# Performance work log

Hardware: AMD Instinct MI355X
Metric: run time of the kernel (lower is better)

## Reference

```python
import jax, jax.numpy as jnp
import numpy as np

NUM_HEADS = 4
KEY_DIMS = 32  # c // num_heads


def rel_to_abs(x):
    # x: [B, N, W, 2W-1] relative logits -> [B, N, W, W] absolute logits
    b, n, w, _ = x.shape
    x = jnp.pad(x, ((0, 0), (0, 0), (0, 0), (0, 1)))           # [b,n,w,2w]
    x = x.reshape(b, n, w * 2 * w)
    x = jnp.pad(x, ((0, 0), (0, 0), (0, w - 1)))
    x = x.reshape(b, n, w + 1, 2 * w - 1)
    return x[:, :, :w, w - 1:]


def rel_logits_1d(q, rel_k):
    # q: [B, heads, X, Y, d], rel_k: [2Y-1, d] -> [B, heads, X, X, Y, Y]
    b, nh, xx, yy, d = q.shape
    rl = jnp.einsum('bhxyd,md->bhxym', q, rel_k)               # [b,h,x,y,2y-1]
    rl = rel_to_abs(rl.reshape(b, nh * xx, yy, 2 * yy - 1))    # [b,h*x,y,y]
    rl = rl.reshape(b, nh, xx, 1, yy, yy)
    return jnp.broadcast_to(rl, (b, nh, xx, xx, yy, yy))


def relative_position_bias(pos_q, pos_emb_h, pos_emb_w):
    # pos_q: [B, heads, H, W, d] -> bias [B, heads, H, W, H, W]
    rw = rel_logits_1d(pos_q, pos_emb_w)                        # [b,h,H,H,W,W]
    rw = rw.transpose(0, 1, 2, 4, 3, 5)                         # [b,h,H,W,H,W]
    rh = rel_logits_1d(pos_q.transpose(0, 1, 3, 2, 4), pos_emb_h)  # [b,h,W,W,H,H]
    rh = rh.transpose(0, 1, 4, 2, 5, 3)                         # [b,h,H,W,H,W]
    return rw + rh


def setup_inputs() -> dict:
    key = jax.random.key(0)
    k1, k2, k3, k4 = jax.random.split(key, 4)
    B, H, W, C = 2, 64, 64, 128
    qk_dims = NUM_HEADS * KEY_DIMS  # 128
    out_channels = C
    x = jax.random.normal(k1, (B, H, W, C), dtype=jnp.float32)
    w_qkv = jax.random.normal(k2, (C, 2 * qk_dims + out_channels), dtype=jnp.float32) * 0.05
    pos_emb_h = jax.random.normal(k3, (2 * H - 1, KEY_DIMS), dtype=jnp.float32) * 0.05
    pos_emb_w = jax.random.normal(k4, (2 * W - 1, KEY_DIMS), dtype=jnp.float32) * 0.05
    return {'x': x, 'w_qkv': w_qkv, 'pos_emb_h': pos_emb_h, 'pos_emb_w': pos_emb_w}


def reference(x, w_qkv, pos_emb_h, pos_emb_w):
    B, H, W, C = x.shape
    nh, kd = NUM_HEADS, KEY_DIMS
    qk_dims = nh * kd
    oc = C
    scale = 1.0 / float(kd) ** 0.5

    qkv = jnp.einsum('bhwc,cd->bhwd', x, w_qkv)                 # 1x1 conv, no bias
    q, k, v = jnp.split(qkv, [qk_dims, 2 * qk_dims], axis=-1)
    L = H * W
    q = q.reshape(B, L, nh, kd).transpose(0, 2, 1, 3)           # [B,nh,L,kd]
    k = k.reshape(B, L, nh, kd).transpose(0, 2, 1, 3)           # [B,nh,L,kd]
    v = v.reshape(B, L, nh, oc // nh).transpose(0, 2, 1, 3)     # [B,nh,L,dv]

    pos_q = q.reshape(B, nh, H, W, kd)
    pos = relative_position_bias(pos_q, pos_emb_h, pos_emb_w).reshape(B, nh, L, L)

    scores = jnp.einsum('bnqd,bnkd->bnqk', q, k) * scale + pos  # [B,nh,L,L]
    attn = jax.nn.softmax(scores, axis=-1)
    out = jnp.einsum('bnqk,bnkd->bnqd', attn, v)                # [B,nh,L,dv]
    out = out.transpose(0, 2, 1, 3).reshape(B, H, W, oc)
    return out
```

## Files before the change

### kernel.cpp

```cpp
#include <hip/hip_runtime.h>
#include <hip/hip_bf16.h>
#include <math.h>

#define B_  2
#define NH  4
#define HH  64
#define WW  64
#define KD  32
#define L_  4096
#define BN_ 8
#define LOG2E 1.4426950408889634f
#define KSCALE (0.17677669529663687f * 1.4426950408889634f)
#define FIXED_M 10.0f

typedef float    f32x4  __attribute__((ext_vector_type(4), may_alias));
typedef _Float16 half8  __attribute__((ext_vector_type(8), may_alias));
typedef _Float16 half4  __attribute__((ext_vector_type(4), may_alias));
typedef __fp16   fp16x2 __attribute__((ext_vector_type(2)));
typedef unsigned uint4v __attribute__((ext_vector_type(4), may_alias));

__device__ __forceinline__ float fexp2(float x) {
#if __has_builtin(__builtin_amdgcn_exp2f)
    return __builtin_amdgcn_exp2f(x);
#else
    return __expf(x * 0.69314718056f);
#endif
}

__device__ __forceinline__ unsigned pack2u(float a, float b) {
    fp16x2 t = __builtin_amdgcn_cvt_pkrtz(a, b);
    union { fp16x2 i; unsigned o; } u;
    u.i = t;
    return u.o;
}

__global__ __launch_bounds__(256) void qkv_gemm(const float* __restrict__ x,
                                                const float* __restrict__ w,
                                                _Float16* __restrict__ q_h,
                                                _Float16* __restrict__ k_h,
                                                _Float16* __restrict__ vt_h) {
    __shared__ __align__(16) char smem[34816];
    _Float16* xs  = (_Float16*)smem;
    _Float16* wsT = (_Float16*)(smem + 17408);

    const int mt = blockIdx.x % 128;
    const int nt = blockIdx.x / 128;
    const int m0 = mt * 64, n0 = nt * 64;
    const int tid = threadIdx.x;
    const int wv = tid >> 6, lane = tid & 63;
    const int l16 = lane & 15, quad = lane >> 4;

    #pragma unroll
    for (int i = 0; i < 8; i++) {
        const int idx = i * 256 + tid;
        const int row = idx >> 5, c4 = (idx & 31) * 4;
        const float4 v = *(const float4*)&x[(size_t)(m0 + row) * 128 + c4];
        half4 h;
        h[0] = (_Float16)v.x; h[1] = (_Float16)v.y;
        h[2] = (_Float16)v.z; h[3] = (_Float16)v.w;
        *(half4*)&xs[row * 136 + c4] = h;
    }
    #pragma unroll
    for (int i = 0; i < 8; i++) {
        const int idx = i * 256 + tid;
        const int k = idx >> 4, c4 = (idx & 15) * 4;
        const float4 v = *(const float4*)&w[(size_t)k * 384 + n0 + c4];
        wsT[(c4 + 0) * 136 + k] = (_Float16)v.x;
        wsT[(c4 + 1) * 136 + k] = (_Float16)v.y;
        wsT[(c4 + 2) * 136 + k] = (_Float16)v.z;
        wsT[(c4 + 3) * 136 + k] = (_Float16)v.w;
    }
    __syncthreads();

    f32x4 acc[4] = {{0.f,0.f,0.f,0.f},{0.f,0.f,0.f,0.f},
                    {0.f,0.f,0.f,0.f},{0.f,0.f,0.f,0.f}};
    half8 af[4];
    #pragma unroll
    for (int kc = 0; kc < 4; kc++)
        af[kc] = *(const half8*)&xs[(wv * 16 + l16) * 136 + kc * 32 + quad * 8];
    #pragma unroll
    for (int ns = 0; ns < 4; ns++)
        #pragma unroll
        for (int kc = 0; kc < 4; kc++) {
            const half8 bf = *(const half8*)&wsT[(ns * 16 + l16) * 136 + kc * 32 + quad * 8];
            acc[ns] = __builtin_amdgcn_mfma_f32_16x16x32_f16(af[kc], bf, acc[ns], 0, 0, 0);
        }

    const int which = n0 >> 7;
    const int nc = n0 & 127;
    const int b = m0 >> 12;
    if (which < 2) {
        _Float16* dst = (which == 0) ? q_h : k_h;
        const float mult = (which == 1) ? KSCALE : 1.0f;
        #pragma unroll
        for (int ns = 0; ns < 4; ns++) {
            const int col = nc + ns * 16 + l16;
            const int bn = b * NH + (col >> 5);
            const int d = col & 31;
            #pragma unroll
            for (int r = 0; r < 4; r++) {
                const int l = (m0 & 4095) + wv * 16 + quad * 4 + r;
                dst[((size_t)bn * L_ + l) * 32 + d] = (_Float16)(acc[ns][r] * mult);
            }
        }
    } else {
        __syncthreads();
        float* img = (float*)smem;
        #pragma unroll
        for (int ns = 0; ns < 4; ns++) {
            const int chan = ns * 16 + l16;
            const int h = chan >> 5, d = chan & 31;
            #pragma unroll
            for (int r = 0; r < 4; r++) {
                const int p = wv * 16 + quad * 4 + r;
                const int y = p >> 5, p32 = p & 31;
                const int q4 = (p32 >> 2) & 3;
                const int j = ((p32 >> 4) & 1) * 4 + (p32 & 3);
                const int fidx = h * 2048 + (y * 2 + (d >> 4)) * 512
                               + (q4 * 16 + (d & 15)) * 8 + j;
                img[fidx + (fidx >> 4)] = acc[ns][r];
            }
        }
        __syncthreads();
        const int ktg = (m0 & 4095) >> 6;
        #pragma unroll
        for (int h = 0; h < 2; h++) {
            const int head = (nc >> 5) + h;
            const int bn = b * NH + head;
            const int fbase = h * 2048 + tid * 8;
            const int sbase = fbase + (fbase >> 4);
            half8 o;
            #pragma unroll
            for (int e = 0; e < 8; e++) o[e] = (_Float16)img[sbase + e];
            *(half8*)(vt_h + (size_t)bn * 131072 + ktg * 2048 + tid * 8) = o;
        }
    }
}

__global__ __launch_bounds__(1024) void attn_mfma(
    const _Float16* __restrict__ q_h,
    const _Float16* __restrict__ k_h,
    const _Float16* __restrict__ vt_h,
    const float* __restrict__ emb_h,
    const float* __restrict__ emb_w,
    float* __restrict__ out)
{
    __shared__ __align__(16) char smem[98816];

    const int bi    = blockIdx.x;
    const int bn    = bi & 7;
    const int wpair = bi >> 3;
    const int tid   = threadIdx.x;
    const int wv    = tid >> 6;
    const int kq    = wv >> 2;
    const int qgp   = (wv >> 1) & 1;
    const int wo    = wv & 1;
    const int w1    = wpair * 2 + wo;
    const int lane  = tid & 63;
    const int l16   = lane & 15;
    const int quad  = lane >> 4;
    const int q0A   = (qgp * 2 + 0) * 16;
    const int q0B   = (qgp * 2 + 1) * 16;

    const _Float16* Kbase = k_h  + (size_t)bn * L_ * 32;
    const _Float16* Vtile = vt_h + (size_t)bn * 131072;

    const int cat  = wv & 7;
    const int kqS  = cat & 3;
    const int isVS = cat >> 2;
    const int halfS = wv >> 3;
    const _Float16* gsrc = (isVS ? Vtile : Kbase) + (size_t)kqS * 16 * 2048;
    const _Float16* gs[2];
    int ldsT[2];
    #pragma unroll
    for (int u = 0; u < 2; u++) {
        const int cc = halfS * 2 + u;
        gs[u] = gsrc + cc * 512 + lane * 8;
        ldsT[u] = kqS * 4096 + isVS * 16384 + (isVS
            ? (cc * 1024 + lane * 16)
            : ((cc * 16 + (lane >> 2)) * 64 + (((lane & 3) ^ ((lane >> 3) & 3)) << 4)));
    }

    const uint4v stg0a = *(const uint4v*)gs[0];
    const uint4v stg0b = *(const uint4v*)gs[1];

    float* RwA = (float*)(smem + 65536) + ((qgp * 2 + 0) * 2 + wo) * 1040;
    float* RwB = (float*)(smem + 65536) + ((qgp * 2 + 1) * 2 + wo) * 1040;

    const half8 aq0 = *(const half8*)(q_h +
        (((size_t)bn * L_ + (q0A + l16) * 64 + w1) * 32 + quad * 8));
    const half8 aq1 = *(const half8*)(q_h +
        (((size_t)bn * L_ + (q0B + l16) * 64 + w1) * 32 + quad * 8));

    f32x4 qwT0[4], qwT1[4];
    #pragma unroll
    for (int sub = 0; sub < 4; sub++) {
        const float* ew = emb_w + (size_t)(sub * 16 + l16 - w1 + 63) * 32 + quad * 8;
        const float4 e0 = *(const float4*)ew;
        const float4 e1 = *(const float4*)(ew + 4);
        union { uint4v u; half8 h; } ua;
        ua.u[0] = pack2u(e0.x * LOG2E, e0.y * LOG2E);
        ua.u[1] = pack2u(e0.z * LOG2E, e0.w * LOG2E);
        ua.u[2] = pack2u(e1.x * LOG2E, e1.y * LOG2E);
        ua.u[3] = pack2u(e1.z * LOG2E, e1.w * LOG2E);
        f32x4 z = {-FIXED_M, -FIXED_M, -FIXED_M, -FIXED_M};
        qwT0[sub] = __builtin_amdgcn_mfma_f32_16x16x32_f16(ua.h, aq0, z, 0, 0, 0);
        qwT1[sub] = __builtin_amdgcn_mfma_f32_16x16x32_f16(ua.h, aq1, z, 0, 0, 0);
    }

    #pragma unroll
    for (int ji = 0; ji < 2; ji++) {
        const int jt = kq * 2 + ji;
        const int j = min(jt * 16 + l16, 126);
        const float* eh = emb_h + (size_t)j * 32 + quad * 8;
        const float4 e0 = *(const float4*)eh;
        const float4 e1 = *(const float4*)(eh + 4);
        union { uint4v u; half8 h; } ub;
        ub.u[0] = pack2u(e0.x * LOG2E, e0.y * LOG2E);
        ub.u[1] = pack2u(e0.z * LOG2E, e0.w * LOG2E);
        ub.u[2] = pack2u(e1.x * LOG2E, e1.y * LOG2E);
        ub.u[3] = pack2u(e1.z * LOG2E, e1.w * LOG2E);
        f32x4 z = {0.f, 0.f, 0.f, 0.f};
        const f32x4 C0 = __builtin_amdgcn_mfma_f32_16x16x32_f16(aq0, ub.h, z, 0, 0, 0);
        const f32x4 C1 = __builtin_amdgcn_mfma_f32_16x16x32_f16(aq1, ub.h, z, 0, 0, 0);
        #pragma unroll
        for (int r = 0; r < 4; r++) {
            const int row = quad * 4 + r;
            const int cA = jt * 16 + l16 - 63 + (q0A + row);
            if (cA >= 0 && cA < 64) RwA[row * 65 + cA] = C0[r];
            const int cB = jt * 16 + l16 - 63 + (q0B + row);
            if (cB >= 0 && cB < 64) RwB[row * 65 + cB] = C1[r];
        }
    }

    *(uint4v*)(smem + ldsT[0]) = stg0a;
    *(uint4v*)(smem + ldsT[1]) = stg0b;
    __syncthreads();

    f32x4 O00 = {0.f,0.f,0.f,0.f}, O01 = {0.f,0.f,0.f,0.f};
    f32x4 O10 = {0.f,0.f,0.f,0.f}, O11 = {0.f,0.f,0.f,0.f};
    float la = 0.f, lb = 0.f;
    const float* qh_rowA = RwA + l16 * 65;
    const float* qh_rowB = RwB + l16 * 65;
#if __has_builtin(__builtin_amdgcn_fdot2)
    fp16x2 onep;
    { union { unsigned u; fp16x2 h; } uo; uo.u = pack2u(1.0f, 1.0f); onep = uo.h; }
#endif

    const int swz16 = ((quad ^ ((l16 >> 1) & 3)) << 4);
    const int kOff = kq * 4096 + l16 * 64 + swz16;
    const int vOff = 16384 + kq * 4096 + lane * 16;

    #pragma unroll 2
    for (int t = 0; t < 16; t++) {
        const int cur = t & 1;
        const int tS = (t < 15) ? (t + 1) : 15;
        const uint4v sa = *(const uint4v*)(gs[0] + (size_t)tS * 2048);
        const uint4v sb = *(const uint4v*)(gs[1] + (size_t)tS * 2048);

        const char* kb = smem + cur * 32768 + kOff;
        const char* vb = smem + cur * 32768 + vOff;
        const half8 kf0 = *(const half8*)(kb);
        const half8 kf1 = *(const half8*)(kb + 1024);
        const half8 kf2 = *(const half8*)(kb + 2048);
        const half8 kf3 = *(const half8*)(kb + 3072);
        const half8 va00 = *(const half8*)(vb);
        const half8 va10 = *(const half8*)(vb + 1024);
        const half8 va01 = *(const half8*)(vb + 2048);
        const half8 va11 = *(const half8*)(vb + 3072);

        const f32x4 S00 = __builtin_amdgcn_mfma_f32_16x16x32_f16(kf0, aq0, qwT0[0], 0, 0, 0);
        const f32x4 S01 = __builtin_amdgcn_mfma_f32_16x16x32_f16(kf1, aq0, qwT0[1], 0, 0, 0);
        const f32x4 S02 = __builtin_amdgcn_mfma_f32_16x16x32_f16(kf2, aq0, qwT0[2], 0, 0, 0);
        const f32x4 S03 = __builtin_amdgcn_mfma_f32_16x16x32_f16(kf3, aq0, qwT0[3], 0, 0, 0);
        const f32x4 S10 = __builtin_amdgcn_mfma_f32_16x16x32_f16(kf0, aq1, qwT1[0], 0, 0, 0);
        const f32x4 S11 = __builtin_amdgcn_mfma_f32_16x16x32_f16(kf1, aq1, qwT1[1], 0, 0, 0);
        const f32x4 S12 = __builtin_amdgcn_mfma_f32_16x16x32_f16(kf2, aq1, qwT1[2], 0, 0, 0);
        const f32x4 S13 = __builtin_amdgcn_mfma_f32_16x16x32_f16(kf3, aq1, qwT1[3], 0, 0, 0);

        const int ktc = kq * 16 + t;
        const int ktn = kq * 16 + tS;
        const float qhA = qh_rowA[ktc];
        const float qhB = qh_rowB[ktc];
        (void)ktn;

        union { uint4v u; half8 h; } p0a, p0b;
        {
            const float a0 = fexp2(S00[0] + qhA), a1 = fexp2(S00[1] + qhA);
            const float a2 = fexp2(S00[2] + qhA), a3 = fexp2(S00[3] + qhA);
            const float a4 = fexp2(S01[0] + qhA), a5 = fexp2(S01[1] + qhA);
            const float a6 = fexp2(S01[2] + qhA), a7 = fexp2(S01[3] + qhA);
            p0a.u[0] = pack2u(a0, a1); p0a.u[1] = pack2u(a2, a3);
            p0a.u[2] = pack2u(a4, a5); p0a.u[3] = pack2u(a6, a7);
            const float b0 = fexp2(S02[0] + qhA), b1 = fexp2(S02[1] + qhA);
            const float b2 = fexp2(S02[2] + qhA), b3 = fexp2(S02[3] + qhA);
            const float b4 = fexp2(S03[0] + qhA), b5 = fexp2(S03[1] + qhA);
            const float b6 = fexp2(S03[2] + qhA), b7 = fexp2(S03[3] + qhA);
            p0b.u[0] = pack2u(b0, b1); p0b.u[1] = pack2u(b2, b3);
            p0b.u[2] = pack2u(b4, b5); p0b.u[3] = pack2u(b6, b7);
        }
        union { uint4v u; half8 h; } p1a, p1b;
        {
            const float a0 = fexp2(S10[0] + qhB), a1 = fexp2(S10[1] + qhB);
            const float a2 = fexp2(S10[2] + qhB), a3 = fexp2(S10[3] + qhB);
            const float a4 = fexp2(S11[0] + qhB), a5 = fexp2(S11[1] + qhB);
            const float a6 = fexp2(S11[2] + qhB), a7 = fexp2(S11[3] + qhB);
            p1a.u[0] = pack2u(a0, a1); p1a.u[1] = pack2u(a2, a3);
            p1a.u[2] = pack2u(a4, a5); p1a.u[3] = pack2u(a6, a7);
            const float b0 = fexp2(S12[0] + qhB), b1 = fexp2(S12[1] + qhB);
            const float b2 = fexp2(S12[2] + qhB), b3 = fexp2(S12[3] + qhB);
            const float b4 = fexp2(S13[0] + qhB), b5 = fexp2(S13[1] + qhB);
            const float b6 = fexp2(S13[2] + qhB), b7 = fexp2(S13[3] + qhB);
            p1b.u[0] = pack2u(b0, b1); p1b.u[1] = pack2u(b2, b3);
            p1b.u[2] = pack2u(b4, b5); p1b.u[3] = pack2u(b4, b5);
            p1b.u[2] = pack2u(b4, b5); p1b.u[3] = pack2u(b6, b7);
        }

        O00 = __builtin_amdgcn_mfma_f32_16x16x32_f16(va00, p0a.h, O00, 0, 0, 0);
        O00 = __builtin_amdgcn_mfma_f32_16x16x32_f16(va01, p0b.h, O00, 0, 0, 0);
        O01 = __builtin_amdgcn_mfma_f32_16x16x32_f16(va10, p0a.h, O01, 0, 0, 0);
        O01 = __builtin_amdgcn_mfma_f32_16x16x32_f16(va11, p0b.h, O01, 0, 0, 0);
        O10 = __builtin_amdgcn_mfma_f32_16x16x32_f16(va00, p1a.h, O10, 0, 0, 0);
        O10 = __builtin_amdgcn_mfma_f32_16x16x32_f16(va01, p1b.h, O10, 0, 0, 0);
        O11 = __builtin_amdgcn_mfma_f32_16x16x32_f16(va10, p1a.h, O11, 0, 0, 0);
        O11 = __builtin_amdgcn_mfma_f32_16x16x32_f16(va11, p1b.h, O11, 0, 0, 0);

#if __has_builtin(__builtin_amdgcn_fdot2)
        {
            union { unsigned u; fp16x2 h; } c0, c1, c2, c3;
            c0.u = p0a.u[0]; c1.u = p0a.u[1]; c2.u = p0a.u[2]; c3.u = p0a.u[3];
            la = __builtin_amdgcn_fdot2(c0.h, onep, la, false);
            la = __builtin_amdgcn_fdot2(c1.h, onep, la, false);
            la = __builtin_amdgcn_fdot2(c2.h, onep, la, false);
            la = __builtin_amdgcn_fdot2(c3.h, onep, la, false);
            c0.u = p0b.u[0]; c1.u = p0b.u[1]; c2.u = p0b.u[2]; c3.u = p0b.u[3];
            la = __builtin_amdgcn_fdot2(c0.h, onep, la, false);
            la = __builtin_amdgcn_fdot2(c1.h, onep, la, false);
            la = __builtin_amdgcn_fdot2(c2.h, onep, la, false);
            la = __builtin_amdgcn_fdot2(c3.h, onep, la, false);
            c0.u = p1a.u[0]; c1.u = p1a.u[1]; c2.u = p1a.u[2]; c3.u = p1a.u[3];
            lb = __builtin_amdgcn_fdot2(c0.h, onep, lb, false);
            lb = __builtin_amdgcn_fdot2(c1.h, onep, lb, false);
            lb = __builtin_amdgcn_fdot2(c2.h, onep, lb, false);
            lb = __builtin_amdgcn_fdot2(c3.h, onep, lb, false);
            c0.u = p1b.u[0]; c1.u = p1b.u[1]; c2.u = p1b.u[2]; c3.u = p1b.u[3];
            lb = __builtin_amdgcn_fdot2(c0.h, onep, lb, false);
            lb = __builtin_amdgcn_fdot2(c1.h, onep, lb, false);
            lb = __builtin_amdgcn_fdot2(c2.h, onep, lb, false);
            lb = __builtin_amdgcn_fdot2(c3.h, onep, lb, false);
        }
#endif

        __builtin_amdgcn_sched_barrier(0);
        *(uint4v*)(smem + (cur ^ 1) * 32768 + ldsT[0]) = sa;
        *(uint4v*)(smem + (cur ^ 1) * 32768 + ldsT[1]) = sb;
        __syncthreads();
    }

    la += __shfl_xor(la, 16);
    la += __shfl_xor(la, 32);
    lb += __shfl_xor(lb, 16);
    lb += __shfl_xor(lb, 32);

    __syncthreads();
    float (*mO)[32][17] = (float(*)[32][17])smem;
    float* mL = (float*)(smem + 69632);
    const int slot0 = wv * 2 + 0;
    const int slot1 = wv * 2 + 1;
    #pragma unroll
    for (int r = 0; r < 4; r++) {
        mO[slot0][quad * 4 + r][l16]      = O00[r];
        mO[slot0][16 + quad * 4 + r][l16] = O01[r];
        mO[slot1][quad * 4 + r][l16]      = O10[r];
        mO[slot1][16 + quad * 4 + r][l16] = O11[r];
    }
    if (quad == 0) {
        mL[slot0 * 16 + l16] = la;
        mL[slot1 * 16 + l16] = lb;
    }
    __syncthreads();

    const int wo_o = tid >> 9;
    const int rest = tid & 511;
    const int h1   = rest >> 3;
    const int dg   = rest & 7;
    const int qg_o = h1 >> 4, ql = h1 & 15;
    const int qgp_o = qg_o >> 1, g_o = qg_o & 1;
    float denom = 0.f;
    float4 o = {0.f, 0.f, 0.f, 0.f};
    #pragma unroll
    for (int kqe = 0; kqe < 4; kqe++) {
        const int s = ((kqe * 4 + qgp_o * 2 + wo_o) << 1) + g_o;
        denom += mL[s * 16 + ql];
        o.x += mO[s][dg * 4 + 0][ql];
        o.y += mO[s][dg * 4 + 1][ql];
        o.z += mO[s][dg * 4 + 2][ql];
        o.w += mO[s][dg * 4 + 3][ql];
    }
    const float inv = 1.0f / denom;
    o.x *= inv; o.y *= inv; o.z *= inv; o.w *= inv;
    const int head = bn & 3, bb = bn >> 2;
    const int w1o = wpair * 2 + wo_o;
    *(float4*)&out[(((size_t)bb * 64 + h1) * 64 + w1o) * 128 + head * 32 + dg * 4] = o;
}

extern "C" void kernel_launch(void* const* d_in, const int* in_sizes, int n_in,
                              void* d_out, int out_size, void* d_ws, size_t ws_size,
                              hipStream_t stream) {
    const float* x     = (const float*)d_in[0];
    const float* w_qkv = (const float*)d_in[1];
    const float* emb_h = (const float*)d_in[2];
    const float* emb_w = (const float*)d_in[3];
    float* out = (float*)d_out;

    _Float16* q_h  = (_Float16*)d_ws;
    _Float16* k_h  = q_h + (size_t)BN_ * L_ * KD;
    _Float16* vt_h = k_h + (size_t)BN_ * L_ * KD;

    qkv_gemm<<<768, 256, 0, stream>>>(x, w_qkv, q_h, k_h, vt_h);
    attn_mfma<<<256, 1024, 0, stream>>>(q_h, k_h, vt_h, emb_h, emb_w, out);
}
```

Before: 99.60 us.

## Stage two key tiles per LDS buffer to halve barriers per loop

Doubles the LDS staging buffers so each iteration loads and processes two K/V tiles. This halves the number of __syncthreads and loop iterations, going from 16 to 8. The relative-width bias table switches from a padded stride of 65 to an XOR-swizzled stride of 64. LDS use grows to 160KB per block, which stays within MI355X's larger LDS but raises register pressure from holding four prefetch vectors per thread.

```diff
diff --git a/kernel.cpp b/kernel.cpp
--- a/kernel.cpp
+++ b/kernel.cpp
@@ -145,7 +145,7 @@
     const float* __restrict__ emb_w,
     float* __restrict__ out)
 {
-    __shared__ __align__(16) char smem[98816];
+    __shared__ __align__(16) char smem[163840];
 
     const int bi    = blockIdx.x;
     const int bn    = bi & 7;
@@ -170,22 +170,25 @@
     const int isVS = cat >> 2;
     const int halfS = wv >> 3;
     const _Float16* gsrc = (isVS ? Vtile : Kbase) + (size_t)kqS * 16 * 2048;
-    const _Float16* gs[2];
-    int ldsT[2];
-    #pragma unroll
-    for (int u = 0; u < 2; u++) {
-        const int cc = halfS * 2 + u;
-        gs[u] = gsrc + cc * 512 + lane * 8;
-        ldsT[u] = kqS * 4096 + isVS * 16384 + (isVS
-            ? (cc * 1024 + lane * 16)
-            : ((cc * 16 + (lane >> 2)) * 64 + (((lane & 3) ^ ((lane >> 3) & 3)) << 4)));
-    }
-
-    const uint4v stg0a = *(const uint4v*)gs[0];
-    const uint4v stg0b = *(const uint4v*)gs[1];
-
-    float* RwA = (float*)(smem + 65536) + ((qgp * 2 + 0) * 2 + wo) * 1040;
-    float* RwB = (float*)(smem + 65536) + ((qgp * 2 + 1) * 2 + wo) * 1040;
+    const _Float16* gs[4];
+    int ldsT[4];
+    #pragma unroll
+    for (int u = 0; u < 4; u++) {
+        const int cc = halfS * 4 + u;
+        const int tile = cc >> 2;
+        const int c4   = cc & 3;
+        gs[u] = gsrc + tile * 2048 + c4 * 512 + lane * 8;
+        ldsT[u] = kqS * 8192 + isVS * 32768 + tile * 4096 + (isVS
+            ? (c4 * 1024 + lane * 16)
+            : ((c4 * 16 + (lane >> 2)) * 64 + (((lane & 3) ^ ((lane >> 3) & 3)) << 4)));
+    }
+
+    uint4v stg0[4];
+    #pragma unroll
+    for (int u = 0; u < 4; u++) stg0[u] = *(const uint4v*)gs[u];
+
+    float* RwA = (float*)(smem + 131072) + ((qgp * 2 + 0) * 2 + wo) * 1024;
+    float* RwB = (float*)(smem + 131072) + ((qgp * 2 + 1) * 2 + wo) * 1024;
 
     const half8 aq0 = *(const half8*)(q_h +
         (((size_t)bn * L_ + (q0A + l16) * 64 + w1) * 32 + quad * 8));
@@ -227,133 +230,134 @@
         for (int r = 0; r < 4; r++) {
             const int row = quad * 4 + r;
             const int cA = jt * 16 + l16 - 63 + (q0A + row);
-            if (cA >= 0 && cA < 64) RwA[row * 65 + cA] = C0[r];
+            if (cA >= 0 && cA < 64) RwA[row * 64 + (cA ^ row)] = C0[r];
             const int cB = jt * 16 + l16 - 63 + (q0B + row);
-            if (cB >= 0 && cB < 64) RwB[row * 65 + cB] = C1[r];
-        }
-    }
-
-    *(uint4v*)(smem + ldsT[0]) = stg0a;
-    *(uint4v*)(smem + ldsT[1]) = stg0b;
+            if (cB >= 0 && cB < 64) RwB[row * 64 + (cB ^ row)] = C1[r];
+        }
+    }
+
+    #pragma unroll
+    for (int u = 0; u < 4; u++) *(uint4v*)(smem + ldsT[u]) = stg0[u];
     __syncthreads();
 
     f32x4 O00 = {0.f,0.f,0.f,0.f}, O01 = {0.f,0.f,0.f,0.f};
     f32x4 O10 = {0.f,0.f,0.f,0.f}, O11 = {0.f,0.f,0.f,0.f};
     float la = 0.f, lb = 0.f;
-    const float* qh_rowA = RwA + l16 * 65;
-    const float* qh_rowB = RwB + l16 * 65;
 #if __has_builtin(__builtin_amdgcn_fdot2)
     fp16x2 onep;
     { union { unsigned u; fp16x2 h; } uo; uo.u = pack2u(1.0f, 1.0f); onep = uo.h; }
 #endif
 
     const int swz16 = ((quad ^ ((l16 >> 1) & 3)) << 4);
-    const int kOff = kq * 4096 + l16 * 64 + swz16;
-    const int vOff = 16384 + kq * 4096 + lane * 16;
-
-    #pragma unroll 2
-    for (int t = 0; t < 16; t++) {
+    const int kOff = kq * 8192 + l16 * 64 + swz16;
+    const int vOff = 32768 + kq * 8192 + lane * 16;
+
+    #pragma unroll 1
+    for (int t = 0; t < 8; t++) {
         const int cur = t & 1;
-        const int tS = (t < 15) ? (t + 1) : 15;
-        const uint4v sa = *(const uint4v*)(gs[0] + (size_t)tS * 2048);
-        const uint4v sb = *(const uint4v*)(gs[1] + (size_t)tS * 2048);
-
-        const char* kb = smem + cur * 32768 + kOff;
-        const char* vb = smem + cur * 32768 + vOff;
-        const half8 kf0 = *(const half8*)(kb);
-        const half8 kf1 = *(const half8*)(kb + 1024);
-        const half8 kf2 = *(const half8*)(kb + 2048);
-        const half8 kf3 = *(const half8*)(kb + 3072);
-        const half8 va00 = *(const half8*)(vb);
-        const half8 va10 = *(const half8*)(vb + 1024);
-        const half8 va01 = *(const half8*)(vb + 2048);
-        const half8 va11 = *(const half8*)(vb + 3072);
-
-        const f32x4 S00 = __builtin_amdgcn_mfma_f32_16x16x32_f16(kf0, aq0, qwT0[0], 0, 0, 0);
-        const f32x4 S01 = __builtin_amdgcn_mfma_f32_16x16x32_f16(kf1, aq0, qwT0[1], 0, 0, 0);
-        const f32x4 S02 = __builtin_amdgcn_mfma_f32_16x16x32_f16(kf2, aq0, qwT0[2], 0, 0, 0);
-        const f32x4 S03 = __builtin_amdgcn_mfma_f32_16x16x32_f16(kf3, aq0, qwT0[3], 0, 0, 0);
-        const f32x4 S10 = __builtin_amdgcn_mfma_f32_16x16x32_f16(kf0, aq1, qwT1[0], 0, 0, 0);
-        const f32x4 S11 = __builtin_amdgcn_mfma_f32_16x16x32_f16(kf1, aq1, qwT1[1], 0, 0, 0);
-        const f32x4 S12 = __builtin_amdgcn_mfma_f32_16x16x32_f16(kf2, aq1, qwT1[2], 0, 0, 0);
-        const f32x4 S13 = __builtin_amdgcn_mfma_f32_16x16x32_f16(kf3, aq1, qwT1[3], 0, 0, 0);
-
-        const int ktc = kq * 16 + t;
-        const int ktn = kq * 16 + tS;
-        const float qhA = qh_rowA[ktc];
-        const float qhB = qh_rowB[ktc];
-        (void)ktn;
-
-        union { uint4v u; half8 h; } p0a, p0b;
-        {
-            const float a0 = fexp2(S00[0] + qhA), a1 = fexp2(S00[1] + qhA);
-            const float a2 = fexp2(S00[2] + qhA), a3 = fexp2(S00[3] + qhA);
-            const float a4 = fexp2(S01[0] + qhA), a5 = fexp2(S01[1] + qhA);
-            const float a6 = fexp2(S01[2] + qhA), a7 = fexp2(S01[3] + qhA);
-            p0a.u[0] = pack2u(a0, a1); p0a.u[1] = pack2u(a2, a3);
-            p0a.u[2] = pack2u(a4, a5); p0a.u[3] = pack2u(a6, a7);
-            const float b0 = fexp2(S02[0] + qhA), b1 = fexp2(S02[1] + qhA);
-            const float b2 = fexp2(S02[2] + qhA), b3 = fexp2(S02[3] + qhA);
-            const float b4 = fexp2(S03[0] + qhA), b5 = fexp2(S03[1] + qhA);
-            const float b6 = fexp2(S03[2] + qhA), b7 = fexp2(S03[3] + qhA);
-            p0b.u[0] = pack2u(b0, b1); p0b.u[1] = pack2u(b2, b3);
-            p0b.u[2] = pack2u(b4, b5); p0b.u[3] = pack2u(b6, b7);
-        }
-        union { uint4v u; half8 h; } p1a, p1b;
-        {
-            const float a0 = fexp2(S10[0] + qhB), a1 = fexp2(S10[1] + qhB);
-            const float a2 = fexp2(S10[2] + qhB), a3 = fexp2(S10[3] + qhB);
-            const float a4 = fexp2(S11[0] + qhB), a5 = fexp2(S11[1] + qhB);
-            const float a6 = fexp2(S11[2] + qhB), a7 = fexp2(S11[3] + qhB);
-            p1a.u[0] = pack2u(a0, a1); p1a.u[1] = pack2u(a2, a3);
-            p1a.u[2] = pack2u(a4, a5); p1a.u[3] = pack2u(a6, a7);
-            const float b0 = fexp2(S12[0] + qhB), b1 = fexp2(S12[1] + qhB);
-            const float b2 = fexp2(S12[2] + qhB), b3 = fexp2(S12[3] + qhB);
-            const float b4 = fexp2(S13[0] + qhB), b5 = fexp2(S13[1] + qhB);
-            const float b6 = fexp2(S13[2] + qhB), b7 = fexp2(S13[3] + qhB);
-            p1b.u[0] = pack2u(b0, b1); p1b.u[1] = pack2u(b2, b3);
-            p1b.u[2] = pack2u(b4, b5); p1b.u[3] = pack2u(b4, b5);
-            p1b.u[2] = pack2u(b4, b5); p1b.u[3] = pack2u(b6, b7);
-        }
-
-        O00 = __builtin_amdgcn_mfma_f32_16x16x32_f16(va00, p0a.h, O00, 0, 0, 0);
-        O00 = __builtin_amdgcn_mfma_f32_16x16x32_f16(va01, p0b.h, O00, 0, 0, 0);
-        O01 = __builtin_amdgcn_mfma_f32_16x16x32_f16(va10, p0a.h, O01, 0, 0, 0);
-        O01 = __builtin_amdgcn_mfma_f32_16x16x32_f16(va11, p0b.h, O01, 0, 0, 0);
-        O10 = __builtin_amdgcn_mfma_f32_16x16x32_f16(va00, p1a.h, O10, 0, 0, 0);
-        O10 = __builtin_amdgcn_mfma_f32_16x16x32_f16(va01, p1b.h, O10, 0, 0, 0);
-        O11 = __builtin_amdgcn_mfma_f32_16x16x32_f16(va10, p1a.h, O11, 0, 0, 0);
-        O11 = __builtin_amdgcn_mfma_f32_16x16x32_f16(va11, p1b.h, O11, 0, 0, 0);
+        const int tS = (t < 7) ? (t + 1) : 7;
+        uint4v sa[4];
+        #pragma unroll
+        for (int u = 0; u < 4; u++)
+            sa[u] = *(const uint4v*)(gs[u] + (size_t)tS * 4096);
+
+        #pragma unroll
+        for (int tt = 0; tt < 2; tt++) {
+            const char* kb = smem + cur * 65536 + kOff + tt * 4096;
+            const char* vb = smem + cur * 65536 + vOff + tt * 4096;
+            const half8 kf0 = *(const half8*)(kb);
+            const half8 kf1 = *(const half8*)(kb + 1024);
+            const half8 kf2 = *(const half8*)(kb + 2048);
+            const half8 kf3 = *(const half8*)(kb + 3072);
+            const half8 va00 = *(const half8*)(vb);
+            const half8 va10 = *(const half8*)(vb + 1024);
+            const half8 va01 = *(const half8*)(vb + 2048);
+            const half8 va11 = *(const half8*)(vb + 3072);
+
+            const f32x4 S00 = __builtin_amdgcn_mfma_f32_16x16x32_f16(kf0, aq0, qwT0[0], 0, 0, 0);
+            const f32x4 S01 = __builtin_amdgcn_mfma_f32_16x16x32_f16(kf1, aq0, qwT0[1], 0, 0, 0);
+            const f32x4 S02 = __builtin_amdgcn_mfma_f32_16x16x32_f16(kf2, aq0, qwT0[2], 0, 0, 0);
+            const f32x4 S03 = __builtin_amdgcn_mfma_f32_16x16x32_f16(kf3, aq0, qwT0[3], 0, 0, 0);
+            const f32x4 S10 = __builtin_amdgcn_mfma_f32_16x16x32_f16(kf0, aq1, qwT1[0], 0, 0, 0);
+            const f32x4 S11 = __builtin_amdgcn_mfma_f32_16x16x32_f16(kf1, aq1, qwT1[1], 0, 0, 0);
+            const f32x4 S12 = __builtin_amdgcn_mfma_f32_16x16x32_f16(kf2, aq1, qwT1[2], 0, 0, 0);
+            const f32x4 S13 = __builtin_amdgcn_mfma_f32_16x16x32_f16(kf3, aq1, qwT1[3], 0, 0, 0);
+
+            const int kt = kq * 16 + 2 * t + tt;
+            const float qhA = RwA[l16 * 64 + (kt ^ l16)];
+            const float qhB = RwB[l16 * 64 + (kt ^ l16)];
+
+            union { uint4v u; half8 h; } p0a, p0b;
+            {
+                const float a0 = fexp2(S00[0] + qhA), a1 = fexp2(S00[1] + qhA);
+                const float a2 = fexp2(S00[2] + qhA), a3 = fexp2(S00[3] + qhA);
+                const float a4 = fexp2(S01[0] + qhA), a5 = fexp2(S01[1] + qhA);
+                const float a6 = fexp2(S01[2] + qhA), a7 = fexp2(S01[3] + qhA);
+                p0a.u[0] = pack2u(a0, a1); p0a.u[1] = pack2u(a2, a3);
+                p0a.u[2] = pack2u(a4, a5); p0a.u[3] = pack2u(a6, a7);
+                const float b0 = fexp2(S02[0] + qhA), b1 = fexp2(S02[1] + qhA);
+                const float b2 = fexp2(S02[2] + qhA), b3 = fexp2(S02[3] + qhA);
+                const float b4 = fexp2(S03[0] + qhA), b5 = fexp2(S03[1] + qhA);
+                const float b6 = fexp2(S03[2] + qhA), b7 = fexp2(S03[3] + qhA);
+                p0b.u[0] = pack2u(b0, b1); p0b.u[1] = pack2u(b2, b3);
+                p0b.u[2] = pack2u(b4, b5); p0b.u[3] = pack2u(b6, b7);
+            }
+            union { uint4v u; half8 h; } p1a, p1b;
+            {
+                const float a0 = fexp2(S10[0] + qhB), a1 = fexp2(S10[1] + qhB);
+                const float a2 = fexp2(S10[2] + qhB), a3 = fexp2(S10[3] + qhB);
+                const float a4 = fexp2(S11[0] + qhB), a5 = fexp2(S11[1] + qhB);
+                const float a6 = fexp2(S11[2] + qhB), a7 = fexp2(S11[3] + qhB);
+                p1a.u[0] = pack2u(a0, a1); p1a.u[1] = pack2u(a2, a3);
+                p1a.u[2] = pack2u(a4, a5); p1a.u[3] = pack2u(a6, a7);
+                const float b0 = fexp2(S12[0] + qhB), b1 = fexp2(S12[1] + qhB);
+                const float b2 = fexp2(S12[2] + qhB), b3 = fexp2(S12[3] + qhB);
+                const float b4 = fexp2(S13[0] + qhB), b5 = fexp2(S13[1] + qhB);
+                const float b6 = fexp2(S13[2] + qhB), b7 = fexp2(S13[3] + qhB);
+                p1b.u[0] = pack2u(b0, b1); p1b.u[1] = pack2u(b2, b3);
+                p1b.u[2] = pack2u(b4, b5); p1b.u[3] = pack2u(b6, b7);
+            }
+
+            O00 = __builtin_amdgcn_mfma_f32_16x16x32_f16(va00, p0a.h, O00, 0, 0, 0);
+            O00 = __builtin_amdgcn_mfma_f32_16x16x32_f16(va01, p0b.h, O00, 0, 0, 0);
+            O01 = __builtin_amdgcn_mfma_f32_16x16x32_f16(va10, p0a.h, O01, 0, 0, 0);
+            O01 = __builtin_amdgcn_mfma_f32_16x16x32_f16(va11, p0b.h, O01, 0, 0, 0);
+            O10 = __builtin_amdgcn_mfma_f32_16x16x32_f16(va00, p1a.h, O10, 0, 0, 0);
+            O10 = __builtin_amdgcn_mfma_f32_16x16x32_f16(va01, p1b.h, O10, 0, 0, 0);
+            O11 = __builtin_amdgcn_mfma_f32_16x16x32_f16(va10, p1a.h, O11, 0, 0, 0);
+            O11 = __builtin_amdgcn_mfma_f32_16x16x32_f16(va11, p1b.h, O11, 0, 0, 0);
 
 #if __has_builtin(__builtin_amdgcn_fdot2)
-        {
-            union { unsigned u; fp16x2 h; } c0, c1, c2, c3;
-            c0.u = p0a.u[0]; c1.u = p0a.u[1]; c2.u = p0a.u[2]; c3.u = p0a.u[3];
-            la = __builtin_amdgcn_fdot2(c0.h, onep, la, false);
-            la = __builtin_amdgcn_fdot2(c1.h, onep, la, false);
-            la = __builtin_amdgcn_fdot2(c2.h, onep, la, false);
-            la = __builtin_amdgcn_fdot2(c3.h, onep, la, false);
-            c0.u = p0b.u[0]; c1.u = p0b.u[1]; c2.u = p0b.u[2]; c3.u = p0b.u[3];
-            la = __builtin_amdgcn_fdot2(c0.h, onep, la, false);
-            la = __builtin_amdgcn_fdot2(c1.h, onep, la, false);
-            la = __builtin_amdgcn_fdot2(c2.h, onep, la, false);
-            la = __builtin_amdgcn_fdot2(c3.h, onep, la, false);
-            c0.u = p1a.u[0]; c1.u = p1a.u[1]; c2.u = p1a.u[2]; c3.u = p1a.u[3];
-            lb = __builtin_amdgcn_fdot2(c0.h, onep, lb, false);
-            lb = __builtin_amdgcn_fdot2(c1.h, onep, lb, false);
-            lb = __builtin_amdgcn_fdot2(c2.h, onep, lb, false);
-            lb = __builtin_amdgcn_fdot2(c3.h, onep, lb, false);
-            c0.u = p1b.u[0]; c1.u = p1b.u[1]; c2.u = p1b.u[2]; c3.u = p1b.u[3];
-            lb = __builtin_amdgcn_fdot2(c0.h, onep, lb, false);
-            lb = __builtin_amdgcn_fdot2(c1.h, onep, lb, false);
-            lb = __builtin_amdgcn_fdot2(c2.h, onep, lb, false);
-            lb = __builtin_amdgcn_fdot2(c3.h, onep, lb, false);
-        }
+            {
+                union { unsigned u; fp16x2 h; } c0, c1, c2, c3;
+                c0.u = p0a.u[0]; c1.u = p0a.u[1]; c2.u = p0a.u[2]; c3.u = p0a.u[3];
+                la = __builtin_amdgcn_fdot2(c0.h, onep, la, false);
+                la = __builtin_amdgcn_fdot2(c1.h, onep, la, false);
+                la = __builtin_amdgcn_fdot2(c2.h, onep, la, false);
+                la = __builtin_amdgcn_fdot2(c3.h, onep, la, false);
+                c0.u = p0b.u[0]; c1.u = p0b.u[1]; c2.u = p0b.u[2]; c3.u = p0b.u[3];
+                la = __builtin_amdgcn_fdot2(c0.h, onep, la, false);
+                la = __builtin_amdgcn_fdot2(c1.h, onep, la, false);
+                la = __builtin_amdgcn_fdot2(c2.h, onep, la, false);
+                la = __builtin_amdgcn_fdot2(c3.h, onep, la, false);
+                c0.u = p1a.u[0]; c1.u = p1a.u[1]; c2.u = p1a.u[2]; c3.u = p1a.u[3];
+                lb = __builtin_amdgcn_fdot2(c0.h, onep, lb, false);
+                lb = __builtin_amdgcn_fdot2(c1.h, onep, lb, false);
+                lb = __builtin_amdgcn_fdot2(c2.h, onep, lb, false);
+                lb = __builtin_amdgcn_fdot2(c3.h, onep, lb, false);
+                c0.u = p1b.u[0]; c1.u = p1b.u[1]; c2.u = p1b.u[2]; c3.u = p1b.u[3];
+                lb = __builtin_amdgcn_fdot2(c0.h, onep, lb, false);
+                lb = __builtin_amdgcn_fdot2(c1.h, onep, lb, false);
+                lb = __builtin_amdgcn_fdot2(c2.h, onep, lb, false);
+                lb = __builtin_amdgcn_fdot2(c3.h, onep, lb, false);
+            }
 #endif
+        }
 
         __builtin_amdgcn_sched_barrier(0);
-        *(uint4v*)(smem + (cur ^ 1) * 32768 + ldsT[0]) = sa;
-        *(uint4v*)(smem + (cur ^ 1) * 32768 + ldsT[1]) = sb;
+        #pragma unroll
+        for (int u = 0; u < 4; u++)
+            *(uint4v*)(smem + (cur ^ 1) * 65536 + ldsT[u]) = sa[u];
         __syncthreads();
     }
 
```

After: 136.0 us. 1.37x slower.

## Use four-stage LDS ring with prefetch distance two and halve barriers

Applied to the files above, without the earlier changes.

Expands the K/V shared-memory staging from two buffers to a four-buffer ring. Two tiles are preloaded up front, and each iteration prefetches two tiles ahead, so a block barrier is needed only every other iteration. The relative-position bias table moves to a new offset and switches from a padded stride-65 layout to an XOR-swizzled stride-64 layout to avoid bank conflicts. This raises LDS use to 160KB per block, which limits occupancy to one block per CU and adds extra global loads in flight.

```diff
diff --git a/kernel.cpp b/kernel.cpp
--- a/kernel.cpp
+++ b/kernel.cpp
@@ -145,7 +145,7 @@
     const float* __restrict__ emb_w,
     float* __restrict__ out)
 {
-    __shared__ __align__(16) char smem[98816];
+    __shared__ __align__(16) char smem[163840];
 
     const int bi    = blockIdx.x;
     const int bn    = bi & 7;
@@ -181,11 +181,13 @@
             : ((cc * 16 + (lane >> 2)) * 64 + (((lane & 3) ^ ((lane >> 3) & 3)) << 4)));
     }
 
-    const uint4v stg0a = *(const uint4v*)gs[0];
-    const uint4v stg0b = *(const uint4v*)gs[1];
-
-    float* RwA = (float*)(smem + 65536) + ((qgp * 2 + 0) * 2 + wo) * 1040;
-    float* RwB = (float*)(smem + 65536) + ((qgp * 2 + 1) * 2 + wo) * 1040;
+    const uint4v s0a = *(const uint4v*)gs[0];
+    const uint4v s0b = *(const uint4v*)gs[1];
+    const uint4v s1a = *(const uint4v*)(gs[0] + 2048);
+    const uint4v s1b = *(const uint4v*)(gs[1] + 2048);
+
+    float* RwA = (float*)(smem + 131072) + ((qgp * 2 + 0) * 2 + wo) * 1024;
+    float* RwB = (float*)(smem + 131072) + ((qgp * 2 + 1) * 2 + wo) * 1024;
 
     const half8 aq0 = *(const half8*)(q_h +
         (((size_t)bn * L_ + (q0A + l16) * 64 + w1) * 32 + quad * 8));
@@ -227,21 +229,21 @@
         for (int r = 0; r < 4; r++) {
             const int row = quad * 4 + r;
             const int cA = jt * 16 + l16 - 63 + (q0A + row);
-            if (cA >= 0 && cA < 64) RwA[row * 65 + cA] = C0[r];
+            if (cA >= 0 && cA < 64) RwA[row * 64 + (cA ^ row)] = C0[r];
             const int cB = jt * 16 + l16 - 63 + (q0B + row);
-            if (cB >= 0 && cB < 64) RwB[row * 65 + cB] = C1[r];
-        }
-    }
-
-    *(uint4v*)(smem + ldsT[0]) = stg0a;
-    *(uint4v*)(smem + ldsT[1]) = stg0b;
+            if (cB >= 0 && cB < 64) RwB[row * 64 + (cB ^ row)] = C1[r];
+        }
+    }
+
+    *(uint4v*)(smem + ldsT[0]) = s0a;
+    *(uint4v*)(smem + ldsT[1]) = s0b;
+    *(uint4v*)(smem + 32768 + ldsT[0]) = s1a;
+    *(uint4v*)(smem + 32768 + ldsT[1]) = s1b;
     __syncthreads();
 
     f32x4 O00 = {0.f,0.f,0.f,0.f}, O01 = {0.f,0.f,0.f,0.f};
     f32x4 O10 = {0.f,0.f,0.f,0.f}, O11 = {0.f,0.f,0.f,0.f};
     float la = 0.f, lb = 0.f;
-    const float* qh_rowA = RwA + l16 * 65;
-    const float* qh_rowB = RwB + l16 * 65;
 #if __has_builtin(__builtin_amdgcn_fdot2)
     fp16x2 onep;
     { union { unsigned u; fp16x2 h; } uo; uo.u = pack2u(1.0f, 1.0f); onep = uo.h; }
@@ -253,13 +255,13 @@
 
     #pragma unroll 2
     for (int t = 0; t < 16; t++) {
-        const int cur = t & 1;
-        const int tS = (t < 15) ? (t + 1) : 15;
+        const int tS = (t < 14) ? (t + 2) : 15;
         const uint4v sa = *(const uint4v*)(gs[0] + (size_t)tS * 2048);
         const uint4v sb = *(const uint4v*)(gs[1] + (size_t)tS * 2048);
 
-        const char* kb = smem + cur * 32768 + kOff;
-        const char* vb = smem + cur * 32768 + vOff;
+        const char* buf = smem + (t & 3) * 32768;
+        const char* kb = buf + kOff;
+        const char* vb = buf + vOff;
         const half8 kf0 = *(const half8*)(kb);
         const half8 kf1 = *(const half8*)(kb + 1024);
         const half8 kf2 = *(const half8*)(kb + 2048);
@@ -278,11 +280,9 @@
         const f32x4 S12 = __builtin_amdgcn_mfma_f32_16x16x32_f16(kf2, aq1, qwT1[2], 0, 0, 0);
         const f32x4 S13 = __builtin_amdgcn_mfma_f32_16x16x32_f16(kf3, aq1, qwT1[3], 0, 0, 0);
 
-        const int ktc = kq * 16 + t;
-        const int ktn = kq * 16 + tS;
-        const float qhA = qh_rowA[ktc];
-        const float qhB = qh_rowB[ktc];
-        (void)ktn;
+        const int kt = kq * 16 + t;
+        const float qhA = RwA[l16 * 64 + (kt ^ l16)];
+        const float qhB = RwB[l16 * 64 + (kt ^ l16)];
 
         union { uint4v u; half8 h; } p0a, p0b;
         {
@@ -312,7 +312,6 @@
             const float b4 = fexp2(S13[0] + qhB), b5 = fexp2(S13[1] + qhB);
             const float b6 = fexp2(S13[2] + qhB), b7 = fexp2(S13[3] + qhB);
             p1b.u[0] = pack2u(b0, b1); p1b.u[1] = pack2u(b2, b3);
-            p1b.u[2] = pack2u(b4, b5); p1b.u[3] = pack2u(b4, b5);
             p1b.u[2] = pack2u(b4, b5); p1b.u[3] = pack2u(b6, b7);
         }
 
@@ -352,9 +351,10 @@
 #endif
 
         __builtin_amdgcn_sched_barrier(0);
-        *(uint4v*)(smem + (cur ^ 1) * 32768 + ldsT[0]) = sa;
-        *(uint4v*)(smem + (cur ^ 1) * 32768 + ldsT[1]) = sb;
-        __syncthreads();
+        char* wbuf = (char*)smem + ((t + 2) & 3) * 32768;
+        *(uint4v*)(wbuf + ldsT[0]) = sa;
+        *(uint4v*)(wbuf + ldsT[1]) = sb;
+        if (t & 1) __syncthreads();
     }
 
     la += __shfl_xor(la, 16);
```

New measurement: 99.41 us. No clear change (-0.2%).
